# Kernel optimization log

Hardware: AMD Instinct MI355X
Metric: run time of the kernel (lower is better)

Reference implementation:

```python
import jax, jax.numpy as jnp
import numpy as np

IN_CH = [32, 48, 96, 136, 232]
SIZES = [128, 64, 32, 16, 8]
C = 256      # FPN channels (compound_coef=0)
A = 9        # anchors per location
NC = 10      # num_classes
B = 8
BN_EPS = 1e-5


def conv2d(x, w, b, pad):
    # x: [B,Cin,H,W], w: [Cout,Cin,kh,kw]
    y = jax.lax.conv_general_dilated(
        x, w, window_strides=(1, 1), padding=[(pad, pad), (pad, pad)],
        dimension_numbers=("NCHW", "OIHW", "NCHW"))
    return y + b[None, :, None, None]


def bn_eval(x, g, bt, m, v):
    inv = g / jnp.sqrt(v + BN_EPS)
    return x * inv[None, :, None, None] + (bt - m * inv)[None, :, None, None]


def upsample_nearest(x, th, tw):
    fh = th // x.shape[2]
    fw = tw // x.shape[3]
    return jnp.repeat(jnp.repeat(x, fh, axis=2), fw, axis=3)


def run_head(feats, w1, b1, g, bt, m, v, w2, b2, out_dim):
    outs = []
    for f in feats:
        h = jax.nn.relu(bn_eval(conv2d(f, w1, b1, 1), g, bt, m, v))
        h = conv2d(h, w2, b2, 0)                       # [B, A*out_dim, H, W]
        Bb, _, H, W = h.shape
        h = h.transpose(0, 2, 3, 1).reshape(Bb, H * W * A, out_dim)
        outs.append(h)
    return jnp.concatenate(outs, axis=1)               # [B, total_anchors, out_dim]


def _forward(f1, f2, f3, f4, f5,
             lat_w1, lat_w2, lat_w3, lat_w4, lat_w5, lat_b,
             fpn_w, fpn_b,
             cls_w1, cls_b1, cls_g, cls_bt, cls_m, cls_v, cls_w2, cls_b2,
             reg_w1, reg_b1, reg_g, reg_bt, reg_m, reg_v, reg_w2, reg_b2):
    feats = [f1, f2, f3, f4, f5]
    lat_ws = [lat_w1, lat_w2, lat_w3, lat_w4, lat_w5]
    # lateral 1x1 convs
    laterals = [conv2d(feats[i], lat_ws[i], lat_b[i], 0) for i in range(5)]
    # top-down pathway with nearest upsampling
    for i in range(4, 0, -1):
        th, tw = laterals[i - 1].shape[2], laterals[i - 1].shape[3]
        laterals[i - 1] = laterals[i - 1] + upsample_nearest(laterals[i], th, tw)
    # 3x3 fpn convs
    fpn_feats = [conv2d(laterals[i], fpn_w[i], fpn_b[i], 1) for i in range(5)]
    cls = run_head(fpn_feats, cls_w1, cls_b1, cls_g, cls_bt, cls_m, cls_v, cls_w2, cls_b2, NC)
    reg = run_head(fpn_feats, reg_w1, reg_b1, reg_g, reg_bt, reg_m, reg_v, reg_w2, reg_b2, 4)
    return jnp.concatenate([reg, cls], axis=2)          # [B, total_anchors, 4+NC]


def setup_inputs() -> dict:
    key = jax.random.key(0)
    ks = jax.random.split(key, 16)
    d = {}
    for i, (ch, s) in enumerate(zip(IN_CH, SIZES)):
        d[f"f{i+1}"] = jax.random.normal(ks[i], (B, ch, s, s), jnp.float32)
    for i, ch in enumerate(IN_CH):
        std = float(np.sqrt(2.0 / C))
        d[f"lat_w{i+1}"] = jax.random.normal(ks[5 + i], (C, ch, 1, 1), jnp.float32) * std
    d["lat_b"] = jnp.zeros((5, C), jnp.float32)
    d["fpn_w"] = jax.random.normal(ks[10], (5, C, C, 3, 3), jnp.float32) * float(np.sqrt(2.0 / (9 * C)))
    d["fpn_b"] = jnp.zeros((5, C), jnp.float32)
    d["cls_w1"] = jax.random.normal(ks[11], (C, C, 3, 3), jnp.float32) * float(np.sqrt(2.0 / (9 * C)))
    d["cls_b1"] = jnp.zeros((C,), jnp.float32)
    d["cls_g"] = jnp.ones((C,), jnp.float32)
    d["cls_bt"] = jnp.zeros((C,), jnp.float32)
    d["cls_m"] = jnp.zeros((C,), jnp.float32)
    d["cls_v"] = jnp.ones((C,), jnp.float32)
    d["cls_w2"] = jax.random.normal(ks[12], (A * NC, C, 1, 1), jnp.float32) * float(np.sqrt(2.0 / (A * NC)))
    d["cls_b2"] = jnp.zeros((A * NC,), jnp.float32)
    d["reg_w1"] = jax.random.normal(ks[13], (C, C, 3, 3), jnp.float32) * float(np.sqrt(2.0 / (9 * C)))
    d["reg_b1"] = jnp.zeros((C,), jnp.float32)
    d["reg_g"] = jnp.ones((C,), jnp.float32)
    d["reg_bt"] = jnp.zeros((C,), jnp.float32)
    d["reg_m"] = jnp.zeros((C,), jnp.float32)
    d["reg_v"] = jnp.ones((C,), jnp.float32)
    d["reg_w2"] = jax.random.normal(ks[14], (A * 4, C, 1, 1), jnp.float32) * float(np.sqrt(2.0 / (A * 4)))
    d["reg_b2"] = jnp.zeros((A * 4,), jnp.float32)
    return d


def reference(f1, f2, f3, f4, f5,
              lat_w1, lat_w2, lat_w3, lat_w4, lat_w5, lat_b,
              fpn_w, fpn_b,
              cls_w1, cls_b1, cls_g, cls_bt, cls_m, cls_v, cls_w2, cls_b2,
              reg_w1, reg_b1, reg_g, reg_bt, reg_m, reg_v, reg_w2, reg_b2):
    return _forward(f1, f2, f3, f4, f5,
                    lat_w1, lat_w2, lat_w3, lat_w4, lat_w5, lat_b,
                    fpn_w, fpn_b,
                    cls_w1, cls_b1, cls_g, cls_bt, cls_m, cls_v, cls_w2, cls_b2,
                    reg_w1, reg_b1, reg_g, reg_bt, reg_m, reg_v, reg_w2, reg_b2)
```

## Files before the change

kernel.cpp:

```cpp
#include <hip/hip_runtime.h>


typedef unsigned short ush;
typedef __attribute__((ext_vector_type(8))) short v8s;
typedef __attribute__((ext_vector_type(4))) float v4f;

constexpr int TOTAL_ANCH = 196416;

#define VMW(n) asm volatile("s_waitcnt vmcnt(" #n ")" ::: "memory")
#define LGW()  asm volatile("s_waitcnt lgkmcnt(0)" ::: "memory")

__device__ __forceinline__ ush f2bf(float x) {
    unsigned u = __builtin_bit_cast(unsigned, x);
    u += 0x7FFFu + ((u >> 16) & 1u);
    return (ush)(u >> 16);
}
__device__ __forceinline__ float bf2f(ush h) {
    unsigned u = ((unsigned)h) << 16;
    return __builtin_bit_cast(float, u);
}
__device__ __forceinline__ void splitf(float x, ush& hi, ush& lo) {
    hi = f2bf(x);
    lo = f2bf(x - bf2f(hi));
}

__device__ __forceinline__ void gl_lds16(const ush* g, short* l) {
    __builtin_amdgcn_global_load_lds(
        (const __attribute__((address_space(1))) unsigned*)(const void*)g,
        (__attribute__((address_space(3))) unsigned*)l, 16, 0, 0);
}

struct Lvl3 {
    const ush* xh; const ush* xl;
    ush* yh; ush* yl;
    const float* bias;
    int wofs, logS, logHW, bstart;
};
struct Tab3 { Lvl3 l[4]; };

struct LvlS {
    const ush* xh; const ush* xl;
    int abase, logHW, bstart, ibase;
};
struct TabS { LvlS l[4]; };

#define MFMA3(AH, AL, BH, BL, ACC)                                            \
    ACC = __builtin_amdgcn_mfma_f32_16x16x32_bf16(AH, BH, ACC, 0, 0, 0);      \
    ACC = __builtin_amdgcn_mfma_f32_16x16x32_bf16(AH, BL, ACC, 0, 0, 0);      \
    ACC = __builtin_amdgcn_mfma_f32_16x16x32_bf16(AL, BH, ACC, 0, 0, 0);

#define RDA(BP, IB)                                                           \
    _Pragma("unroll")                                                         \
    for (int i = 0; i < 4; ++i) {                                             \
        a_h[i] = *(const v8s*)((BP) + abA + ((IB) + i) * 512);                \
        a_l[i] = *(const v8s*)((BP) + abA + 8192 + ((IB) + i) * 512);         \
    }

#define RDB(BP, JB)                                                           \
    _Pragma("unroll")                                                         \
    for (int j = 0; j < 2; ++j) {                                             \
        b_h[j] = *(const v8s*)((BP) + abB + ((JB) + j) * 512);                \
        b_l[j] = *(const v8s*)((BP) + abB + 8192 + ((JB) + j) * 512);         \
    }

#define PHASE(IB, JB)                                                         \
    LGW();                                                                    \
    __builtin_amdgcn_sched_barrier(0);                                        \
    __builtin_amdgcn_s_setprio(1);                                            \
    _Pragma("unroll")                                                         \
    for (int j = 0; j < 2; ++j) {                                             \
        _Pragma("unroll")                                                     \
        for (int i = 0; i < 4; ++i) {                                         \
            MFMA3(a_h[i], a_l[i], b_h[j], b_l[j], acc[(IB) + i][(JB) + j]);   \
        }                                                                     \
    }                                                                         \
    __builtin_amdgcn_s_setprio(0);

template <int OM, bool BNR>
__global__ __launch_bounds__(512, 2)
void conv3g(Tab3 T,
            const ush* __restrict__ Wh, const ush* __restrict__ Wl,
            const float* __restrict__ bng, const float* __restrict__ bnb,
            const float* __restrict__ bnm, const float* __restrict__ bnv)
{
    constexpr int K = 2304, KC = 72;
    constexpr int BUFS = 32768;

    const int nwg = gridDim.x;
    const int flat = blockIdx.x;
    const int xcd = flat & 7, sidx = flat >> 3;
    const int q = nwg >> 3, r8 = nwg & 7;
    const int nf = (xcd < r8 ? xcd * (q + 1) : r8 * (q + 1) + (xcd - r8) * q) + sidx;

    int li = 0;
    if (nf >= T.l[1].bstart) li = 1;
    if (nf >= T.l[2].bstart) li = 2;
    if (nf >= T.l[3].bstart) li = 3;
    const int logS = T.l[li].logS, logHW = T.l[li].logHW;
    const int S = 1 << logS, HW = 1 << logHW, P = S + 2;
    const ush* __restrict__ Xh = T.l[li].xh;
    const ush* __restrict__ Xl = T.l[li].xl;
    ush* __restrict__ Yh = T.l[li].yh;
    ush* __restrict__ Yl = T.l[li].yl;
    const float* __restrict__ bias = T.l[li].bias;
    const int wofs = T.l[li].wofs;
    const int n0 = (nf - T.l[li].bstart) * 256;

    __shared__ __align__(16) short lds[2][BUFS];

    const int tid = threadIdx.x;
    const int lane = tid & 63, w = tid >> 6;
    const int wm = w & 1, wn = w >> 1;
    const int l15 = lane & 15, l4 = lane >> 4;
    const int lr = lane >> 2, ls = lane & 3;
    const int sw = ls ^ ((lr >> 1) & 3);

    const int role = w >> 1, part = w & 1;
    const ush* gsrc = role == 0 ? Wh + wofs : role == 1 ? Wl + wofs
                    : role == 2 ? Xh : Xl;
    const int poff = role * 8192 + part * 4096;

    int sb[8];
    if (role < 2) {
#pragma unroll
        for (int t = 0; t < 8; ++t)
            sb[t] = (part * 128 + t * 16 + lr) * K + sw * 8;
    } else {
#pragma unroll
        for (int t = 0; t < 8; ++t) {
            const int p = n0 + part * 128 + t * 16 + lr;
            const int bb = p >> logHW, hw = p & (HW - 1);
            const int oh = hw >> logS, ow = hw & (S - 1);
            sb[t] = ((bb * P + oh + 1) * P + ow + 1) * 256 + sw * 8;
        }
    }

    auto stage = [&](int u, int c) {
        short* db = &lds[0][0] + u * BUFS + poff;
        int coff;
        if (role < 2) coff = c * 32;
        else {
            const int rs = c >> 3;
            const int rr = (rs * 11) >> 5;
            const int ss = rs - 3 * rr;
            coff = ((rr - 1) * P + (ss - 1)) * 256 + (c & 7) * 32;
        }
#pragma unroll
        for (int t = 0; t < 8; ++t)
            gl_lds16(gsrc + (sb[t] + coff), db + t * 512);
    };

    const int slr = (l4 ^ ((l15 >> 1) & 3)) * 8;
    const int abA = (wm * 128 + l15) * 32 + slr;
    const int abB = 16384 + (wn * 64 + l15) * 32 + slr;

    v4f acc[8][4] = {};
    v8s a_h[4], a_l[4], b_h[2], b_l[2];

    stage(0, 0);
    VMW(0);
    __builtin_amdgcn_sched_barrier(0);
    __builtin_amdgcn_s_barrier();

    int cur = 0;
    for (int c = 0; c < KC; ++c) {
        if (c + 1 < KC) stage(cur ^ 1, c + 1);
        const short* bp = &lds[0][0] + cur * BUFS;

        RDA(bp, 0); RDB(bp, 0);
        PHASE(0, 0);
        RDA(bp, 4);
        PHASE(4, 0);
        RDB(bp, 2);
        PHASE(4, 2);
        RDA(bp, 0);
        PHASE(0, 2);

        if (c + 1 < KC) VMW(0);
        __builtin_amdgcn_sched_barrier(0);
        __builtin_amdgcn_s_barrier();
        cur ^= 1;
    }

#pragma unroll
    for (int i = 0; i < 8; ++i) {
        const int co = wm * 128 + i * 16 + l4 * 4;
        float sc[4], sh[4];
#pragma unroll
        for (int e = 0; e < 4; ++e) {
            if (BNR) {
                const float inv = bng[co + e] * rsqrtf(bnv[co + e] + 1e-5f);
                sc[e] = inv;
                sh[e] = (bias[co + e] - bnm[co + e]) * inv + bnb[co + e];
            } else { sc[e] = 1.f; sh[e] = bias[co + e]; }
        }
#pragma unroll
        for (int j = 0; j < 4; ++j) {
            const int ncol = n0 + wn * 64 + j * 16 + l15;
            const int b  = ncol >> logHW;
            const int hw = ncol & (HW - 1);
            float val[4];
#pragma unroll
            for (int e = 0; e < 4; ++e) {
                float x = acc[i][j][e] * sc[e] + sh[e];
                if (BNR) x = fmaxf(x, 0.f);
                val[e] = x;
            }
            int pidx;
            if (OM == 0) {
                const int oh = hw >> logS, ow = hw & (S - 1);
                pidx = (b * P + oh + 1) * P + ow + 1;
            } else {
                pidx = ncol;
            }
            const int addr = pidx * 256 + co;
            ush hs[4], ls2[4];
#pragma unroll
            for (int e = 0; e < 4; ++e) splitf(val[e], hs[e], ls2[e]);
            *(uint2*)&Yh[addr] = make_uint2(hs[0] | ((unsigned)hs[1] << 16),
                                            hs[2] | ((unsigned)hs[3] << 16));
            *(uint2*)&Yl[addr] = make_uint2(ls2[0] | ((unsigned)ls2[1] << 16),
                                            ls2[2] | ((unsigned)ls2[3] << 16));
        }
    }
}

template <int DD>
__global__ __launch_bounds__(256, 3)
void conv_sf(TabS T, const ush* __restrict__ Wh, const ush* __restrict__ Wl,
             const float* __restrict__ bias, float* __restrict__ out)
{
    constexpr int K = 256, KC = 8, Cout = 9 * DD;
    constexpr int coloff = (DD == 10) ? 4 : 0;

    const int nwg = gridDim.x;
    const int flat = blockIdx.x;
    const int xcd = flat & 7, sidx = flat >> 3;
    const int q = nwg >> 3, r8 = nwg & 7;
    const int nf = (xcd < r8 ? xcd * (q + 1) : r8 * (q + 1) + (xcd - r8) * q) + sidx;

    int li = 0;
    if (nf >= T.l[1].bstart) li = 1;
    if (nf >= T.l[2].bstart) li = 2;
    if (nf >= T.l[3].bstart) li = 3;
    const int logHW = T.l[li].logHW;
    const int HW = 1 << logHW;
    const ush* __restrict__ Xh = T.l[li].xh;
    const ush* __restrict__ Xl = T.l[li].xl;
    const int abase = T.l[li].abase, ibase = T.l[li].ibase;
    const int n0 = (nf - T.l[li].bstart) * 128;

    __shared__ short lds[4][128][32];

    const int tid = threadIdx.x;
    const int lane = tid & 63;
    const int w = tid >> 6;
    const int wm = w & 1, wn = w >> 1;
    const int l15 = lane & 15, l4 = lane >> 4;
    const int lr = lane >> 2, ls = lane & 3;
    const int sw = ls ^ ((lr >> 1) & 3);
    const ush* gsrc = (w == 0) ? Wh : (w == 1) ? Wl : (w == 2) ? Xh : Xl;
    int sb[8];
    if (w < 2) {
#pragma unroll
        for (int t = 0; t < 8; ++t)
            sb[t] = (t * 16 + lr) * K + sw * 8;
    } else {
#pragma unroll
        for (int t = 0; t < 8; ++t)
            sb[t] = (n0 + t * 16 + lr) * 256 + sw * 8;
    }
    short* mypl = &lds[w][0][0];
    const int slA = (l4 ^ ((l15 >> 1) & 3)) * 8;

    v4f acc[4][4] = {};

    for (int c = 0; c < KC; ++c) {
        const int coff = c * 32;
#pragma unroll
        for (int t = 0; t < 8; ++t)
            gl_lds16(gsrc + (sb[t] + coff), mypl + t * 512);

        __syncthreads();

        v8s ah[4], al[4];
#pragma unroll
        for (int i = 0; i < 4; ++i) {
            ah[i] = *(const v8s*)&lds[0][wm * 64 + i * 16 + l15][slA];
            al[i] = *(const v8s*)&lds[1][wm * 64 + i * 16 + l15][slA];
        }
#pragma unroll
        for (int j = 0; j < 4; ++j) {
            const v8s bh = *(const v8s*)&lds[2][wn * 64 + j * 16 + l15][slA];
            const v8s bl = *(const v8s*)&lds[3][wn * 64 + j * 16 + l15][slA];
#pragma unroll
            for (int i = 0; i < 4; ++i) {
                acc[i][j] = __builtin_amdgcn_mfma_f32_16x16x32_bf16(ah[i], bh, acc[i][j], 0, 0, 0);
                acc[i][j] = __builtin_amdgcn_mfma_f32_16x16x32_bf16(ah[i], bl, acc[i][j], 0, 0, 0);
                acc[i][j] = __builtin_amdgcn_mfma_f32_16x16x32_bf16(al[i], bh, acc[i][j], 0, 0, 0);
            }
        }
        __syncthreads();
    }

#pragma unroll
    for (int i = 0; i < 4; ++i) {
        const int co = wm * 64 + i * 16 + l4 * 4;
        float sh[4];
#pragma unroll
        for (int e = 0; e < 4; ++e)
            sh[e] = (co + e < Cout) ? bias[co + e] : 0.f;
#pragma unroll
        for (int j = 0; j < 4; ++j) {
            const int ncol = n0 + wn * 64 + j * 16 + l15;
            const int b  = ncol >> logHW;
            const int hw = ncol & (HW - 1);
#pragma unroll
            for (int e = 0; e < 4; ++e) {
                const int c2 = co + e;
                if (c2 < Cout) {
                    const float val = acc[i][j][e] + sh[e];
                    const int a = c2 / DD, cl = c2 - a * DD;
                    out[(size_t)((b + ibase) * TOTAL_ANCH + abase + hw * 9 + a) * 14
                        + coloff + cl] = val;
                }
            }
        }
    }
}

template <int KS, int OM, bool BNR, int DD>
__global__ __launch_bounds__(256, 3)
void conv_mfma(const ush* __restrict__ Xh, const ush* __restrict__ Xl,
               const ush* __restrict__ Wh, const ush* __restrict__ Wl,
               const float* __restrict__ bias,
               ush* __restrict__ Yh, ush* __restrict__ Yl,
               int K, int logS, int logHW, int Kin)
{
    const int tid = threadIdx.x;

    const int nwg  = gridDim.x * gridDim.y;
    const int flat = blockIdx.y * gridDim.x + blockIdx.x;
    const int xcd = flat & 7, sidx = flat >> 3;
    const int q = nwg >> 3, r8 = nwg & 7;
    const int nf = (xcd < r8 ? xcd * (q + 1) : r8 * (q + 1) + (xcd - r8) * q) + sidx;
    int bx, by;
    if (gridDim.y == 2) { bx = nf >> 1; by = nf & 1; }
    else                { bx = nf;      by = 0;      }

    const int n0  = bx * 128;
    const int co0 = by * 128;
    const int S = 1 << logS, HW = 1 << logHW, P = S + 2;

    __shared__ short lds[4][128][32];

    const int lane = tid & 63;
    const int w = tid >> 6;
    const int wm = w & 1, wn = w >> 1;
    const int l15 = lane & 15, l4 = lane >> 4;

    const int lr = lane >> 2, ls = lane & 3;
    const int sw = ls ^ ((lr >> 1) & 3);
    const ush* gsrc = (w == 0) ? Wh : (w == 1) ? Wl : (w == 2) ? Xh : Xl;
    int sb[8];
    if (w < 2) {
#pragma unroll
        for (int t = 0; t < 8; ++t)
            sb[t] = (co0 + t * 16 + lr) * K + sw * 8;
    } else {
#pragma unroll
        for (int t = 0; t < 8; ++t) {
            const int p = n0 + t * 16 + lr;
            sb[t] = p * Kin + sw * 8;
        }
    }
    short* mypl = &lds[w][0][0];

    const int KC = K >> 5;
    const int slA = (l4 ^ ((l15 >> 1) & 3)) * 8;

    v4f acc[4][4] = {};

    for (int c = 0; c < KC; ++c) {
        const int coff = c * 32;
#pragma unroll
        for (int t = 0; t < 8; ++t)
            gl_lds16(gsrc + (sb[t] + coff), mypl + t * 512);

        __syncthreads();

        v8s ah[4], al[4];
#pragma unroll
        for (int i = 0; i < 4; ++i) {
            ah[i] = *(const v8s*)&lds[0][wm * 64 + i * 16 + l15][slA];
            al[i] = *(const v8s*)&lds[1][wm * 64 + i * 16 + l15][slA];
        }
#pragma unroll
        for (int j = 0; j < 4; ++j) {
            const v8s bh = *(const v8s*)&lds[2][wn * 64 + j * 16 + l15][slA];
            const v8s bl = *(const v8s*)&lds[3][wn * 64 + j * 16 + l15][slA];
#pragma unroll
            for (int i = 0; i < 4; ++i) {
                acc[i][j] = __builtin_amdgcn_mfma_f32_16x16x32_bf16(ah[i], bh, acc[i][j], 0, 0, 0);
                acc[i][j] = __builtin_amdgcn_mfma_f32_16x16x32_bf16(ah[i], bl, acc[i][j], 0, 0, 0);
                acc[i][j] = __builtin_amdgcn_mfma_f32_16x16x32_bf16(al[i], bh, acc[i][j], 0, 0, 0);
            }
        }
        __syncthreads();
    }

#pragma unroll
    for (int i = 0; i < 4; ++i) {
        const int cob = wm * 64 + i * 16 + l4 * 4;
        const int co  = co0 + cob;
        float sh[4];
#pragma unroll
        for (int e = 0; e < 4; ++e) sh[e] = bias[co + e];
#pragma unroll
        for (int j = 0; j < 4; ++j) {
            const int ncol = n0 + wn * 64 + j * 16 + l15;
            const int b  = ncol >> logHW;
            const int hw = ncol & (HW - 1);
            float val[4];
#pragma unroll
            for (int e = 0; e < 4; ++e) val[e] = acc[i][j][e] + sh[e];
            int pidx;
            if (OM == 0) {
                const int oh = hw >> logS, ow = hw & (S - 1);
                pidx = (b * P + oh + 1) * P + ow + 1;
            } else {
                pidx = ncol;
            }
            const int addr = pidx * 256 + co;
            ush hs[4], ls2[4];
#pragma unroll
            for (int e = 0; e < 4; ++e) splitf(val[e], hs[e], ls2[e]);
            *(uint2*)&Yh[addr] = make_uint2(hs[0] | ((unsigned)hs[1] << 16),
                                            hs[2] | ((unsigned)hs[3] << 16));
            *(uint2*)&Yl[addr] = make_uint2(ls2[0] | ((unsigned)ls2[1] << 16),
                                            ls2[2] | ((unsigned)ls2[3] << 16));
        }
    }
}


__global__ void w3_prep(const float* __restrict__ W, ush* __restrict__ wh,
                        ush* __restrict__ wl, int total) {
    const int idx = blockIdx.x * 256 + threadIdx.x;
    if (idx >= total) return;
    const int co5 = idx / 2304;
    const int kk  = idx - co5 * 2304;
    const int rs = kk >> 8, ci = kk & 255;
    splitf(W[(co5 * 256 + ci) * 9 + rs], wh[idx], wl[idx]);
}

__global__ void w1_prep(const float* __restrict__ W, ush* __restrict__ wh,
                        ush* __restrict__ wl, int Cin, int Kp, int Cout, int total) {
    const int idx = blockIdx.x * 256 + threadIdx.x;
    if (idx >= total) return;
    const int co = idx / Kp;
    const int k  = idx - co * Kp;
    const float x = (co < Cout && k < Cin) ? W[co * Cin + k] : 0.f;
    splitf(x, wh[idx], wl[idx]);
}

__global__ void in_prep(const float* __restrict__ f, ush* __restrict__ xh,
                        ush* __restrict__ xl, int Cin, int Kp, int logHW, int total) {
    const int idx = blockIdx.x * 256 + threadIdx.x;
    if (idx >= total) return;
    const int c = idx % Kp;
    const int n = idx / Kp;
    const int b  = n >> logHW;
    const int hw = n & ((1 << logHW) - 1);
    const float x = (c < Cin) ? f[((b * Cin + c) << logHW) + hw] : 0.f;
    splitf(x, xh[idx], xl[idx]);
}

__global__ void upsample_hl(ush* __restrict__ fh, ush* __restrict__ fl,
                            const ush* __restrict__ ch, const ush* __restrict__ cl2,
                            int logSf, int total) {
    const int idx = blockIdx.x * 256 + threadIdx.x;
    if (idx >= total) return;
    const int ci = idx & 255;
    const int r  = idx >> 8;
    const int Sf = 1 << logSf;
    const int wf = r & (Sf - 1);
    const int hf = (r >> logSf) & (Sf - 1);
    const int b  = r >> (2 * logSf);
    const int Pf = Sf + 2, Pc = (Sf >> 1) + 2;
    const int fi = ((b * Pf + hf + 1) * Pf + wf + 1) * 256 + ci;
    const int cx = ((b * Pc + (hf >> 1) + 1) * Pc + (wf >> 1) + 1) * 256 + ci;
    const float x = bf2f(fh[fi]) + bf2f(fl[fi]) + bf2f(ch[cx]) + bf2f(cl2[cx]);
    splitf(x, fh[fi], fl[fi]);
}

__global__ void ring_zero(ush* __restrict__ yh, ush* __restrict__ yl, int S, int total) {
    const int idx = blockIdx.x * 256 + threadIdx.x;
    if (idx >= total) return;
    const int ci = idx & 255;
    const int r  = idx >> 8;
    const int P = S + 2;
    const int ring = 4 * P - 4;
    const int pr = r % ring;
    const int b  = r / ring;
    int ph, pw;
    if (pr < P)            { ph = 0;     pw = pr; }
    else if (pr < 2 * P)   { ph = P - 1; pw = pr - P; }
    else { const int q = pr - 2 * P; ph = 1 + (q >> 1); pw = (q & 1) ? (P - 1) : 0; }
    const int a = ((b * P + ph) * P + pw) * 256 + ci;
    yh[a] = 0; yl[a] = 0;
}


extern "C" void kernel_launch(void* const* d_in, const int* in_sizes, int n_in,
                              void* d_out, int out_size, void* d_ws, size_t ws_size,
                              hipStream_t stream)
{
    const float* f[5];     const float* lat_w[5];
    for (int i = 0; i < 5; ++i) f[i] = (const float*)d_in[i];
    for (int i = 0; i < 5; ++i) lat_w[i] = (const float*)d_in[5 + i];
    const float* lat_b  = (const float*)d_in[10];
    const float* fpn_w  = (const float*)d_in[11];
    const float* fpn_b  = (const float*)d_in[12];
    const float* cls_w1 = (const float*)d_in[13];
    const float* cls_b1 = (const float*)d_in[14];
    const float* cls_g  = (const float*)d_in[15];
    const float* cls_bt = (const float*)d_in[16];
    const float* cls_m  = (const float*)d_in[17];
    const float* cls_v  = (const float*)d_in[18];
    const float* cls_w2 = (const float*)d_in[19];
    const float* cls_b2 = (const float*)d_in[20];
    const float* reg_w1 = (const float*)d_in[21];
    const float* reg_b1 = (const float*)d_in[22];
    const float* reg_g  = (const float*)d_in[23];
    const float* reg_bt = (const float*)d_in[24];
    const float* reg_m  = (const float*)d_in[25];
    const float* reg_v  = (const float*)d_in[26];
    const float* reg_w2 = (const float*)d_in[27];
    const float* reg_b2 = (const float*)d_in[28];

    float* out = (float*)d_out;
    ush*   ws16 = (ush*)d_ws;

    static const int S_[5]     = {128, 64, 32, 16, 8};
    static const int logS_[5]  = {7, 6, 5, 4, 3};
    static const int logHW_[5] = {14, 12, 10, 8, 6};
    static const int HW_[5]    = {16384, 4096, 1024, 256, 64};
    static const int Cin_[5]   = {32, 48, 96, 136, 232};
    static const int Kp_[5]    = {32, 64, 96, 160, 256};
    static const int abase_[5] = {0, 147456, 184320, 193536, 195840};
    constexpr int BIG = 0x7fffffff;

    size_t off = 0;
    auto alloc = [&](size_t elems) {
        ush* p = ws16 + off;
        off += (elems + 63) & ~(size_t)63;
        return p;
    };

    ush *lat_h[5], *lat_l[5];
    for (int i = 0; i < 5; ++i) {
        const int P = S_[i] + 2;
        const size_t e = (size_t)2048 * P * P;
        lat_h[i] = alloc(e); lat_l[i] = alloc(e);
    }
    const size_t lat_bytes = off * sizeof(ush);

    const size_t ARENA_E = (size_t)2 * 4 * 130 * 130 * 256;
    ush* arena = alloc(ARENA_E);

    ush* fw_h = alloc((size_t)5 * 256 * 2304); ush* fw_l = alloc((size_t)5 * 256 * 2304);
    ush* cw_h = alloc(256 * 2304);             ush* cw_l = alloc(256 * 2304);
    ush* rw_h = alloc(256 * 2304);             ush* rw_l = alloc(256 * 2304);
    ush *lw_h[5], *lw_l[5];
    for (int i = 0; i < 5; ++i) { lw_h[i] = alloc(256 * Kp_[i]); lw_l[i] = alloc(256 * Kp_[i]); }
    ush* c2_h = alloc(128 * 256); ush* c2_l = alloc(128 * 256);
    ush* r2_h = alloc(128 * 256); ush* r2_l = alloc(128 * 256);

    hipMemsetAsync(ws16, 0, lat_bytes, stream);

    {
        int t = 5 * 256 * 2304;
        w3_prep<<<dim3((t + 255) / 256), 256, 0, stream>>>(fpn_w, fw_h, fw_l, t);
        t = 256 * 2304;
        w3_prep<<<dim3((t + 255) / 256), 256, 0, stream>>>(cls_w1, cw_h, cw_l, t);
        w3_prep<<<dim3((t + 255) / 256), 256, 0, stream>>>(reg_w1, rw_h, rw_l, t);
        for (int i = 0; i < 5; ++i) {
            t = 256 * Kp_[i];
            w1_prep<<<dim3((t + 255) / 256), 256, 0, stream>>>(lat_w[i], lw_h[i], lw_l[i], Cin_[i], Kp_[i], 256, t);
        }
        t = 128 * 256;
        w1_prep<<<dim3((t + 255) / 256), 256, 0, stream>>>(cls_w2, c2_h, c2_l, 256, 256, 90, t);
        w1_prep<<<dim3((t + 255) / 256), 256, 0, stream>>>(reg_w2, r2_h, r2_l, 256, 256, 36, t);
    }

    for (int i = 0; i < 5; ++i) {
        const int N = 8 * HW_[i];
        const int t = N * Kp_[i];
        ush* xh = arena;
        ush* xl = arena + (size_t)N * Kp_[i];
        in_prep<<<dim3((t + 255) / 256), 256, 0, stream>>>(f[i], xh, xl, Cin_[i], Kp_[i], logHW_[i], t);
        conv_mfma<1, 0, false, 0><<<dim3(N / 128, 2), 256, 0, stream>>>(
            xh, xl, lw_h[i], lw_l[i], lat_b + i * 256,
            lat_h[i], lat_l[i],
            Kp_[i], logS_[i], logHW_[i], Kp_[i]);
    }

    for (int i = 4; i >= 1; --i) {
        const int t = 8 * HW_[i - 1] * 256;
        upsample_hl<<<dim3((t + 255) / 256), 256, 0, stream>>>(
            lat_h[i - 1], lat_l[i - 1], lat_h[i], lat_l[i], logS_[i - 1], t);
    }

    ush *fpn_h4[5], *fpn_l4[5];
    {
        size_t o = 0;
        for (int i = 1; i < 5; ++i) {
            const int P = S_[i] + 2;
            fpn_h4[i] = arena + o; o += (size_t)2048 * P * P;
            fpn_l4[i] = arena + o; o += (size_t)2048 * P * P;
        }
    }
    for (int i = 1; i < 5; ++i) {
        const int P = S_[i] + 2;
        const int rt = 8 * (4 * P - 4) * 256;
        ring_zero<<<dim3((rt + 255) / 256), 256, 0, stream>>>(fpn_h4[i], fpn_l4[i], S_[i], rt);
    }
    static const int bstart4[4] = {0, 128, 160, 168};
    static const int bstartS[4] = {0, 256, 320, 336};

    {
        Tab3 T{};
        for (int k = 0; k < 4; ++k) {
            const int i = k + 1;
            T.l[k] = Lvl3{ lat_h[i], lat_l[i], fpn_h4[i], fpn_l4[i],
                           fpn_b + i * 256, i * 256 * 2304,
                           logS_[i], logHW_[i], bstart4[k] };
        }
        conv3g<0, false><<<dim3(170), 512, 0, stream>>>(
            T, fw_h, fw_l, nullptr, nullptr, nullptr, nullptr);
    }
    {
        Tab3 T{};
        for (int k = 0; k < 4; ++k) {
            const int i = k + 1;
            T.l[k] = Lvl3{ fpn_h4[i], fpn_l4[i], lat_h[i], lat_l[i],
                           cls_b1, 0, logS_[i], logHW_[i], bstart4[k] };
        }
        conv3g<1, true><<<dim3(170), 512, 0, stream>>>(
            T, cw_h, cw_l, cls_g, cls_bt, cls_m, cls_v);
    }
    {
        TabS T{};
        for (int k = 0; k < 4; ++k) {
            const int i = k + 1;
            T.l[k] = LvlS{ lat_h[i], lat_l[i], abase_[i], logHW_[i], bstartS[k], 0 };
        }
        conv_sf<10><<<dim3(340), 256, 0, stream>>>(T, c2_h, c2_l, cls_b2, out);
    }
    {
        Tab3 T{};
        for (int k = 0; k < 4; ++k) {
            const int i = k + 1;
            T.l[k] = Lvl3{ fpn_h4[i], fpn_l4[i], lat_h[i], lat_l[i],
                           reg_b1, 0, logS_[i], logHW_[i], bstart4[k] };
        }
        conv3g<1, true><<<dim3(170), 512, 0, stream>>>(
            T, rw_h, rw_l, reg_g, reg_bt, reg_m, reg_v);
    }
    {
        TabS T{};
        for (int k = 0; k < 4; ++k) {
            const int i = k + 1;
            T.l[k] = LvlS{ lat_h[i], lat_l[i], abase_[i], logHW_[i], bstartS[k], 0 };
        }
        conv_sf<4><<<dim3(340), 256, 0, stream>>>(T, r2_h, r2_l, reg_b2, out);
    }

    {
        const int P = 130;
        const size_t padg = (size_t)4 * P * P * 256;
        const size_t unpg = (size_t)4 * 16384 * 256;
        for (int g = 0; g < 2; ++g) {
            ush* fpn_h = arena;
            ush* fpn_l = arena + padg;
            ush* lat0p_h = lat_h[0] + (size_t)g * padg;
            ush* lat0p_l = lat_l[0] + (size_t)g * padg;
            ush* tmp_h   = lat_h[0] + (size_t)g * unpg;
            ush* tmp_l   = lat_l[0] + (size_t)g * unpg;
            const int rt = 4 * (4 * P - 4) * 256;
            ring_zero<<<dim3((rt + 255) / 256), 256, 0, stream>>>(fpn_h, fpn_l, 128, rt);

            Tab3 T{};
            T.l[0] = Lvl3{ lat0p_h, lat0p_l, fpn_h, fpn_l, fpn_b, 0, 7, 14, 0 };
            for (int k = 1; k < 4; ++k) T.l[k].bstart = BIG;
            conv3g<0, false><<<dim3(256), 512, 0, stream>>>(
                T, fw_h, fw_l, nullptr, nullptr, nullptr, nullptr);

            Tab3 Tc{};
            Tc.l[0] = Lvl3{ fpn_h, fpn_l, tmp_h, tmp_l, cls_b1, 0, 7, 14, 0 };
            for (int k = 1; k < 4; ++k) Tc.l[k].bstart = BIG;
            conv3g<1, true><<<dim3(256), 512, 0, stream>>>(
                Tc, cw_h, cw_l, cls_g, cls_bt, cls_m, cls_v);

            TabS Ts{};
            Ts.l[0] = LvlS{ tmp_h, tmp_l, 0, 14, 0, 4 * g };
            for (int k = 1; k < 4; ++k) Ts.l[k].bstart = BIG;
            conv_sf<10><<<dim3(512), 256, 0, stream>>>(Ts, c2_h, c2_l, cls_b2, out);

            Tab3 Tr{};
            Tr.l[0] = Lvl3{ fpn_h, fpn_l, tmp_h, tmp_l, reg_b1, 0, 7, 14, 0 };
            for (int k = 1; k < 4; ++k) Tr.l[k].bstart = BIG;
            conv3g<1, true><<<dim3(256), 512, 0, stream>>>(
                Tr, rw_h, rw_l, reg_g, reg_bt, reg_m, reg_v);

            TabS Tq{};
            Tq.l[0] = LvlS{ tmp_h, tmp_l, 0, 14, 0, 4 * g };
            for (int k = 1; k < 4; ++k) Tq.l[k].bstart = BIG;
            conv_sf<4><<<dim3(512), 256, 0, stream>>>(Tq, r2_h, r2_l, reg_b2, out);
        }
    }
}
```

Measured before the change: 2.396 ms.

## Interleave split global-to-LDS prefetch with MFMA phases using ping-pong barriers

The 3x3 conv main loop now splits the next chunk's global-to-LDS staging into three pieces, each issued between the LDS fragment reads and the MFMA work of one phase. Workgroup barriers are added around every phase to keep warps in step, ping-pong style. B fragments are kept in four registers so the A fragment is read only twice per chunk instead of three times, which cuts LDS reads. The extra barriers add sync overhead and register pressure, and the non-unrolled staging loop may add scalar overhead.

```diff
diff --git a/kernel.cpp b/kernel.cpp
--- a/kernel.cpp
+++ b/kernel.cpp
@@ -8,7 +8,8 @@
 constexpr int TOTAL_ANCH = 196416;
 
 #define VMW(n) asm volatile("s_waitcnt vmcnt(" #n ")" ::: "memory")
-#define LGW()  asm volatile("s_waitcnt lgkmcnt(0)" ::: "memory")
+#define LGK(n) asm volatile("s_waitcnt lgkmcnt(" #n ")" ::: "memory")
+#define SB0()  __builtin_amdgcn_sched_barrier(0)
 
 __device__ __forceinline__ ush f2bf(float x) {
     unsigned u = __builtin_bit_cast(unsigned, x);
@@ -49,29 +50,28 @@
     ACC = __builtin_amdgcn_mfma_f32_16x16x32_bf16(AH, BL, ACC, 0, 0, 0);      \
     ACC = __builtin_amdgcn_mfma_f32_16x16x32_bf16(AL, BH, ACC, 0, 0, 0);
 
-#define RDA(BP, IB)                                                           \
+#define RDA(H, BP)                                                            \
     _Pragma("unroll")                                                         \
     for (int i = 0; i < 4; ++i) {                                             \
-        a_h[i] = *(const v8s*)((BP) + abA + ((IB) + i) * 512);                \
-        a_l[i] = *(const v8s*)((BP) + abA + 8192 + ((IB) + i) * 512);         \
-    }
-
-#define RDB(BP, JB)                                                           \
+        a_h[i] = *(const v8s*)((BP) + abA + ((H)*4 + i) * 512);               \
+        a_l[i] = *(const v8s*)((BP) + abA + 8192 + ((H)*4 + i) * 512);        \
+    }
+
+#define RDB2(J0, BP)                                                          \
     _Pragma("unroll")                                                         \
     for (int j = 0; j < 2; ++j) {                                             \
-        b_h[j] = *(const v8s*)((BP) + abB + ((JB) + j) * 512);                \
-        b_l[j] = *(const v8s*)((BP) + abB + 8192 + ((JB) + j) * 512);         \
-    }
-
-#define PHASE(IB, JB)                                                         \
-    LGW();                                                                    \
-    __builtin_amdgcn_sched_barrier(0);                                        \
+        b_h[(J0)+j] = *(const v8s*)((BP) + abB + ((J0)+j) * 512);             \
+        b_l[(J0)+j] = *(const v8s*)((BP) + abB + 8192 + ((J0)+j) * 512);      \
+    }
+
+#define MF24(IB, J0)                                                          \
     __builtin_amdgcn_s_setprio(1);                                            \
     _Pragma("unroll")                                                         \
     for (int j = 0; j < 2; ++j) {                                             \
         _Pragma("unroll")                                                     \
         for (int i = 0; i < 4; ++i) {                                         \
-            MFMA3(a_h[i], a_l[i], b_h[j], b_l[j], acc[(IB) + i][(JB) + j]);   \
+            MFMA3(a_h[i], a_l[i], b_h[(J0)+j], b_l[(J0)+j],                   \
+                  acc[(IB)+i][(J0)+j]);                                       \
         }                                                                     \
     }                                                                         \
     __builtin_amdgcn_s_setprio(0);
@@ -135,7 +135,7 @@
         }
     }
 
-    auto stage = [&](int u, int c) {
+    auto stage_g = [&](int u, int c, int t0, int nt) {
         short* db = &lds[0][0] + u * BUFS + poff;
         int coff;
         if (role < 2) coff = c * 32;
@@ -145,8 +145,7 @@
             const int ss = rs - 3 * rr;
             coff = ((rr - 1) * P + (ss - 1)) * 256 + (c & 7) * 32;
         }
-#pragma unroll
-        for (int t = 0; t < 8; ++t)
+        for (int t = t0; t < t0 + nt; ++t)
             gl_lds16(gsrc + (sb[t] + coff), db + t * 512);
     };
 
@@ -155,29 +154,45 @@
     const int abB = 16384 + (wn * 64 + l15) * 32 + slr;
 
     v4f acc[8][4] = {};
-    v8s a_h[4], a_l[4], b_h[2], b_l[2];
-
-    stage(0, 0);
+    v8s a_h[4], a_l[4];
+    v8s b_h[4], b_l[4];
+
+    stage_g(0, 0, 0, 8);
     VMW(0);
-    __builtin_amdgcn_sched_barrier(0);
+    SB0();
     __builtin_amdgcn_s_barrier();
 
     int cur = 0;
     for (int c = 0; c < KC; ++c) {
-        if (c + 1 < KC) stage(cur ^ 1, c + 1);
+        const bool pf = (c + 1) < KC;
         const short* bp = &lds[0][0] + cur * BUFS;
-
-        RDA(bp, 0); RDB(bp, 0);
-        PHASE(0, 0);
-        RDA(bp, 4);
-        PHASE(4, 0);
-        RDB(bp, 2);
-        PHASE(4, 2);
-        RDA(bp, 0);
-        PHASE(0, 2);
-
-        if (c + 1 < KC) VMW(0);
-        __builtin_amdgcn_sched_barrier(0);
+        const int nxt = cur ^ 1;
+
+        RDA(0, bp); RDB2(0, bp);
+        if (pf) stage_g(nxt, c + 1, 0, 2);
+        __builtin_amdgcn_s_barrier();
+        LGK(0); SB0();
+        MF24(0, 0);
+        __builtin_amdgcn_s_barrier();
+
+        RDB2(2, bp);
+        if (pf) stage_g(nxt, c + 1, 2, 2);
+        __builtin_amdgcn_s_barrier();
+        LGK(0); SB0();
+        MF24(0, 2);
+        __builtin_amdgcn_s_barrier();
+
+        RDA(1, bp);
+        if (pf) stage_g(nxt, c + 1, 4, 4);
+        __builtin_amdgcn_s_barrier();
+        LGK(0); SB0();
+        MF24(4, 2);
+        __builtin_amdgcn_s_barrier();
+
+        SB0();
+        MF24(4, 0);
+        if (pf) VMW(0);
+        SB0();
         __builtin_amdgcn_s_barrier();
         cur ^= 1;
     }
```

Result: no change. 2.421 ms (+1.0%).

## Deepen conv3g pipeline with two-stage global prefetch and register double-buffered fragments

Applied to the files above, without the earlier changes.

The 3x3 conv GEMM main loop now keeps two global-to-LDS stages in flight instead of one. Matrix fragments are double-buffered in registers, so LDS reads for the next k-chunk are issued while the MFMAs of the current chunk run, and only one barrier remains per iteration. This is meant to hide both global-load latency and LDS-read latency behind MFMA work. In exchange it holds more fragment registers live, which risks register pressure or spills under the 512-thread, 2-block launch bounds.

```diff
diff --git a/kernel.cpp b/kernel.cpp
--- a/kernel.cpp
+++ b/kernel.cpp
@@ -8,7 +8,8 @@
 constexpr int TOTAL_ANCH = 196416;
 
 #define VMW(n) asm volatile("s_waitcnt vmcnt(" #n ")" ::: "memory")
-#define LGW()  asm volatile("s_waitcnt lgkmcnt(0)" ::: "memory")
+#define LGK(n) asm volatile("s_waitcnt lgkmcnt(" #n ")" ::: "memory")
+#define SB0()  __builtin_amdgcn_sched_barrier(0)
 
 __device__ __forceinline__ ush f2bf(float x) {
     unsigned u = __builtin_bit_cast(unsigned, x);
@@ -49,29 +50,38 @@
     ACC = __builtin_amdgcn_mfma_f32_16x16x32_bf16(AH, BL, ACC, 0, 0, 0);      \
     ACC = __builtin_amdgcn_mfma_f32_16x16x32_bf16(AL, BH, ACC, 0, 0, 0);
 
-#define RDA(BP, IB)                                                           \
+#define RDA0(BP)                                                              \
     _Pragma("unroll")                                                         \
     for (int i = 0; i < 4; ++i) {                                             \
-        a_h[i] = *(const v8s*)((BP) + abA + ((IB) + i) * 512);                \
-        a_l[i] = *(const v8s*)((BP) + abA + 8192 + ((IB) + i) * 512);         \
-    }
-
-#define RDB(BP, JB)                                                           \
+        a0h[i] = *(const v8s*)((BP) + abA + i * 512);                         \
+        a0l[i] = *(const v8s*)((BP) + abA + 8192 + i * 512);                  \
+    }
+#define RDA1(BP)                                                              \
+    _Pragma("unroll")                                                         \
+    for (int i = 0; i < 4; ++i) {                                             \
+        a1h[i] = *(const v8s*)((BP) + abA + (4 + i) * 512);                   \
+        a1l[i] = *(const v8s*)((BP) + abA + 8192 + (4 + i) * 512);            \
+    }
+#define RDB01(BP)                                                             \
     _Pragma("unroll")                                                         \
     for (int j = 0; j < 2; ++j) {                                             \
-        b_h[j] = *(const v8s*)((BP) + abB + ((JB) + j) * 512);                \
-        b_l[j] = *(const v8s*)((BP) + abB + 8192 + ((JB) + j) * 512);         \
-    }
-
-#define PHASE(IB, JB)                                                         \
-    LGW();                                                                    \
-    __builtin_amdgcn_sched_barrier(0);                                        \
+        b0h[j] = *(const v8s*)((BP) + abB + j * 512);                         \
+        b0l[j] = *(const v8s*)((BP) + abB + 8192 + j * 512);                  \
+    }
+#define RDB23(BP)                                                             \
+    _Pragma("unroll")                                                         \
+    for (int j = 0; j < 2; ++j) {                                             \
+        b1h[j] = *(const v8s*)((BP) + abB + (2 + j) * 512);                   \
+        b1l[j] = *(const v8s*)((BP) + abB + 8192 + (2 + j) * 512);            \
+    }
+
+#define MF24(AH, AL, BH, BL, IB, JB)                                          \
     __builtin_amdgcn_s_setprio(1);                                            \
     _Pragma("unroll")                                                         \
     for (int j = 0; j < 2; ++j) {                                             \
         _Pragma("unroll")                                                     \
         for (int i = 0; i < 4; ++i) {                                         \
-            MFMA3(a_h[i], a_l[i], b_h[j], b_l[j], acc[(IB) + i][(JB) + j]);   \
+            MFMA3(AH[i], AL[i], BH[j], BL[j], acc[(IB)+i][(JB)+j]);           \
         }                                                                     \
     }                                                                         \
     __builtin_amdgcn_s_setprio(0);
@@ -135,7 +145,7 @@
         }
     }
 
-    auto stage = [&](int u, int c) {
+    auto stage_g = [&](int u, int c) {
         short* db = &lds[0][0] + u * BUFS + poff;
         int coff;
         if (role < 2) coff = c * 32;
@@ -155,30 +165,47 @@
     const int abB = 16384 + (wn * 64 + l15) * 32 + slr;
 
     v4f acc[8][4] = {};
-    v8s a_h[4], a_l[4], b_h[2], b_l[2];
-
-    stage(0, 0);
-    VMW(0);
-    __builtin_amdgcn_sched_barrier(0);
+    v8s a0h[4], a0l[4];
+    v8s a1h[4], a1l[4];
+    v8s b0h[2], b0l[2];
+    v8s b1h[2], b1l[2];
+
+    stage_g(0, 0);
+    stage_g(1, 1);
+    VMW(8); SB0();
     __builtin_amdgcn_s_barrier();
+    SB0();
+    {
+        const short* bp = &lds[0][0];
+        RDA0(bp); RDB01(bp);
+    }
 
     int cur = 0;
     for (int c = 0; c < KC; ++c) {
-        if (c + 1 < KC) stage(cur ^ 1, c + 1);
-        const short* bp = &lds[0][0] + cur * BUFS;
-
-        RDA(bp, 0); RDB(bp, 0);
-        PHASE(0, 0);
-        RDA(bp, 4);
-        PHASE(4, 0);
-        RDB(bp, 2);
-        PHASE(4, 2);
-        RDA(bp, 0);
-        PHASE(0, 2);
-
-        if (c + 1 < KC) VMW(0);
-        __builtin_amdgcn_sched_barrier(0);
+        const short* bp  = &lds[0][0] + cur * BUFS;
+        const short* bpn = &lds[0][0] + (cur ^ 1) * BUFS;
+        const bool p1 = (c + 1) < KC;
+        const bool p2 = (c + 2) < KC;
+
+        LGK(0); SB0();
+        RDB23(bp); RDA1(bp);
+        MF24(a0h, a0l, b0h, b0l, 0, 0);
+
+        LGK(8); SB0();
+        MF24(a0h, a0l, b1h, b1l, 0, 2);
+
+        LGK(0); SB0();
+        VMW(0); SB0();
         __builtin_amdgcn_s_barrier();
+        SB0();
+
+        if (p1) { RDA0(bpn); }
+        if (p2) stage_g(cur, c + 2);
+        MF24(a1h, a1l, b1h, b1l, 4, 2);
+
+        MF24(a1h, a1l, b0h, b0l, 4, 0);
+        if (p1) { RDB01(bpn); }
+
         cur ^= 1;
     }
 
```

Result: no change. 2.381 ms (-0.6%).
